# Performance work log

Hardware: AMD Instinct MI355X
Metric: run time of the kernel (lower is better)

Reference implementation:

```python
import jax, jax.numpy as jnp
import numpy as np

ENC_DIM, DEC_DIM, JOINT_DIM, VOCAB = 512, 640, 512, 1024
B, T, U = 8, 256, 64


def setup_inputs() -> dict:
    key = jax.random.key(0)
    ks = jax.random.split(key, 8)
    s_enc = 1.0 / np.sqrt(ENC_DIM)
    s_dec = 1.0 / np.sqrt(DEC_DIM)
    s_out = 1.0 / np.sqrt(2 * JOINT_DIM)
    return {
        "enc_out": jax.random.normal(ks[0], (B, T, ENC_DIM), jnp.float32),
        "pred_out": jax.random.normal(ks[1], (B, U, DEC_DIM), jnp.float32),
        "W_enc": jax.random.uniform(ks[2], (JOINT_DIM, ENC_DIM), jnp.float32, -s_enc, s_enc),
        "b_enc": jax.random.uniform(ks[3], (JOINT_DIM,), jnp.float32, -s_enc, s_enc),
        "W_pred": jax.random.uniform(ks[4], (JOINT_DIM, DEC_DIM), jnp.float32, -s_dec, s_dec),
        "b_pred": jax.random.uniform(ks[5], (JOINT_DIM,), jnp.float32, -s_dec, s_dec),
        "W_out": jax.random.uniform(ks[6], (VOCAB, 2 * JOINT_DIM), jnp.float32, -s_out, s_out),
        "b_out": jax.random.uniform(ks[7], (VOCAB,), jnp.float32, -s_out, s_out),
    }


def reference(enc_out, pred_out, W_enc, b_enc, W_pred, b_pred, W_out, b_out):
    # Dropout is identity in eval mode. fc_out on cat([enc_exp, pred_exp]) is
    # mathematically identical to splitting W_out in half and summing two
    # broadcast projections (avoids materializing the [B,T,U,2J] tensor).
    J = W_enc.shape[0]
    e = jnp.einsum('bte,je->btj', enc_out, W_enc) + b_enc    # [B,T,J]
    p = jnp.einsum('bud,jd->buj', pred_out, W_pred) + b_pred  # [B,U,J]
    W1, W2 = W_out[:, :J], W_out[:, J:]
    out = (jnp.einsum('btj,vj->btv', e, W1)[:, :, None, :]
           + jnp.einsum('buj,vj->buv', p, W2)[:, None, :, :]
           + b_out)                                           # [B,T,U,V]
    return out
```

## Files before the change

kernel.cpp:

```cpp
#include <hip/hip_runtime.h>

typedef float f4 __attribute__((ext_vector_type(4)));
typedef float f32x4 __attribute__((ext_vector_type(4)));
typedef short bf16x8 __attribute__((ext_vector_type(8)));
typedef unsigned short u16x8 __attribute__((ext_vector_type(8)));

static __device__ __forceinline__ unsigned short f2bf(float f) {
    unsigned int x = __builtin_bit_cast(unsigned int, f);
    x = (x + 0x7fffu + ((x >> 16) & 1u)) >> 16;
    return (unsigned short)x;
}
static __device__ __forceinline__ float bf2f(unsigned short h) {
    unsigned int x = ((unsigned int)h) << 16;
    return __builtin_bit_cast(float, x);
}

static __device__ __forceinline__ void gll16(const unsigned short* g, unsigned short* l) {
    __builtin_amdgcn_global_load_lds(
        (__attribute__((address_space(1))) void*)(g),
        (__attribute__((address_space(3))) void*)(l), 16, 0, 0);
}

static __device__ __forceinline__ int fragoff(int r, int s) {
    return r * 32 + ((s ^ ((r >> 1) & 3)) << 3);
}

struct GJobF {
    const float *A, *W;
    int lda, ldw;
    const float* bias;
    unsigned short *Ch, *Cl;
    int N, K, nbx;
};

__global__ __launch_bounds__(256, 3) void gemmcvt64(
    GJobF j0, GJobF j1, int nblk0, int nblk1,
    const float* __restrict__ Wo, unsigned short* __restrict__ Wo_h,
    unsigned short* __restrict__ Wo_l, int nWo8)
{
    __shared__ unsigned short lds[2][4][64 * 32];

    const int bid = blockIdx.x;
    const int tid = threadIdx.x;

    if (bid >= nblk0 + nblk1) {
        const int nblkc = (int)gridDim.x - nblk0 - nblk1;
        for (int g = (bid - nblk0 - nblk1) * 256 + tid; g < nWo8; g += nblkc * 256) {
            const int idx = g * 8;
            f4 a = *(const f4*)(Wo + idx);
            f4 b = *(const f4*)(Wo + idx + 4);
            u16x8 hv, lv;
            float s[8] = { a.x, a.y, a.z, a.w, b.x, b.y, b.z, b.w };
            #pragma unroll
            for (int i = 0; i < 8; ++i) {
                unsigned short h = f2bf(s[i]);
                hv[i] = h;
                lv[i] = f2bf(s[i] - bf2f(h));
            }
            *(u16x8*)(Wo_h + idx) = hv;
            *(u16x8*)(Wo_l + idx) = lv;
        }
        return;
    }

    const bool first = bid < nblk0;
    const GJobF J = first ? j0 : j1;
    const int local = first ? bid : bid - nblk0;
    const int m0 = (local % J.nbx) * 64;
    const int n0 = (local / J.nbx) * 64;

    const int lane = tid & 63;
    const int wid  = tid >> 6;
    const int wr   = wid >> 1, wc = wid & 1;
    const int lrow = lane & 15;
    const int s    = lane >> 4;

    const int row  = tid >> 2, slot = tid & 3;
    const int woff = fragoff(row, slot);
    const float* pA = J.A + (size_t)(m0 + row) * J.lda + slot * 8;
    const float* pW = J.W + (size_t)(n0 + row) * J.ldw + slot * 8;

    f4 ra0, ra1, rw0, rw1;

#define LOADREGS(k0) do { \
    ra0 = *(const f4*)(pA + (k0));     ra1 = *(const f4*)(pA + (k0) + 4); \
    rw0 = *(const f4*)(pW + (k0));     rw1 = *(const f4*)(pW + (k0) + 4); \
} while (0)

#define CVTWRITE(buf) do { \
    u16x8 ha, la, hw, lw; \
    float sa[8] = { ra0.x, ra0.y, ra0.z, ra0.w, ra1.x, ra1.y, ra1.z, ra1.w }; \
    float sw[8] = { rw0.x, rw0.y, rw0.z, rw0.w, rw1.x, rw1.y, rw1.z, rw1.w }; \
    _Pragma("unroll") \
    for (int i = 0; i < 8; ++i) { \
        unsigned short h = f2bf(sa[i]); \
        ha[i] = h; la[i] = f2bf(sa[i] - bf2f(h)); \
        h = f2bf(sw[i]); \
        hw[i] = h; lw[i] = f2bf(sw[i] - bf2f(h)); \
    } \
    *(u16x8*)&lds[buf][0][woff] = ha; \
    *(u16x8*)&lds[buf][1][woff] = la; \
    *(u16x8*)&lds[buf][2][woff] = hw; \
    *(u16x8*)&lds[buf][3][woff] = lw; \
} while (0)

    f32x4 acc[2][2];
    #pragma unroll
    for (int i = 0; i < 2; ++i)
        #pragma unroll
        for (int j = 0; j < 2; ++j) acc[i][j] = (f32x4){0.f, 0.f, 0.f, 0.f};

    const int nt = J.K / 32;

    LOADREGS(0);
    CVTWRITE(0);
    __syncthreads();

    int cur = 0;
    for (int t = 0; t < nt; ++t) {
        if (t + 1 < nt) LOADREGS((t + 1) * 32);

        bf16x8 ah[2], al[2], wh[2], wl[2];
        #pragma unroll
        for (int i = 0; i < 2; ++i) {
            const int ra = wr * 32 + i * 16 + lrow;
            const int rw = wc * 32 + i * 16 + lrow;
            ah[i] = *(const bf16x8*)&lds[cur][0][fragoff(ra, s)];
            al[i] = *(const bf16x8*)&lds[cur][1][fragoff(ra, s)];
            wh[i] = *(const bf16x8*)&lds[cur][2][fragoff(rw, s)];
            wl[i] = *(const bf16x8*)&lds[cur][3][fragoff(rw, s)];
        }
        #pragma unroll
        for (int i = 0; i < 2; ++i)
            #pragma unroll
            for (int j = 0; j < 2; ++j) {
                acc[i][j] = __builtin_amdgcn_mfma_f32_16x16x32_bf16(ah[i], wh[j], acc[i][j], 0, 0, 0);
                acc[i][j] = __builtin_amdgcn_mfma_f32_16x16x32_bf16(ah[i], wl[j], acc[i][j], 0, 0, 0);
                acc[i][j] = __builtin_amdgcn_mfma_f32_16x16x32_bf16(al[i], wh[j], acc[i][j], 0, 0, 0);
            }

        if (t + 1 < nt) {
            CVTWRITE(cur ^ 1);
            __syncthreads();
            cur ^= 1;
        }
    }
#undef LOADREGS
#undef CVTWRITE

    #pragma unroll
    for (int i = 0; i < 2; ++i) {
        const int rbase = m0 + wr * 32 + i * 16 + (lane >> 4) * 4;
        #pragma unroll
        for (int j = 0; j < 2; ++j) {
            const int col = n0 + wc * 32 + j * 16 + (lane & 15);
            const float bv = J.bias[col];
            #pragma unroll
            for (int r = 0; r < 4; ++r) {
                float v = acc[i][j][r] + bv;
                size_t off = (size_t)(rbase + r) * J.N + col;
                unsigned short h = f2bf(v);
                J.Ch[off] = h;
                J.Cl[off] = f2bf(v - bf2f(h));
            }
        }
    }
}

struct GJob {
    const unsigned short *Ah, *Al, *Wh, *Wl;
    int lda, ldw;
    const float* bias;
    float* Cf;
    int N, K, nbx;
};

__global__ __launch_bounds__(256, 3) void gemm64(GJob j0, GJob j1, int nblk0)
{
    __shared__ unsigned short lds[2][4][64 * 32];

    const bool first = (int)blockIdx.x < nblk0;
    const GJob J = first ? j0 : j1;
    const int local = first ? (int)blockIdx.x : (int)blockIdx.x - nblk0;
    const int m0 = (local % J.nbx) * 64;
    const int n0 = (local / J.nbx) * 64;

    const int tid  = threadIdx.x;
    const int lane = tid & 63;
    const int wid  = tid >> 6;
    const int wr   = wid >> 1, wc = wid & 1;
    const int lrow = lane & 15;
    const int s    = lane >> 4;

    const int srow  = wid * 16 + (lane >> 2);
    const int sslot = (lane & 3) ^ ((srow >> 1) & 3);
    const size_t gA = (size_t)(m0 + srow) * J.lda + sslot * 8;
    const size_t gW = (size_t)(n0 + srow) * J.ldw + sslot * 8;

    f32x4 acc[2][2];
    #pragma unroll
    for (int i = 0; i < 2; ++i)
        #pragma unroll
        for (int j = 0; j < 2; ++j) acc[i][j] = (f32x4){0.f, 0.f, 0.f, 0.f};

    const int nt = J.K / 32;

    gll16(J.Ah + gA, &lds[0][0][wid * 512]);
    gll16(J.Al + gA, &lds[0][1][wid * 512]);
    gll16(J.Wh + gW, &lds[0][2][wid * 512]);
    gll16(J.Wl + gW, &lds[0][3][wid * 512]);
    asm volatile("s_waitcnt vmcnt(0)" ::: "memory");
    __syncthreads();

    int cur = 0;
    for (int t = 0; t < nt; ++t) {
        if (t + 1 < nt) {
            const int k0 = (t + 1) * 32;
            gll16(J.Ah + gA + k0, &lds[cur ^ 1][0][wid * 512]);
            gll16(J.Al + gA + k0, &lds[cur ^ 1][1][wid * 512]);
            gll16(J.Wh + gW + k0, &lds[cur ^ 1][2][wid * 512]);
            gll16(J.Wl + gW + k0, &lds[cur ^ 1][3][wid * 512]);
        }

        bf16x8 ah[2], al[2], wh[2], wl[2];
        #pragma unroll
        for (int i = 0; i < 2; ++i) {
            const int ra = wr * 32 + i * 16 + lrow;
            const int rw = wc * 32 + i * 16 + lrow;
            ah[i] = *(const bf16x8*)&lds[cur][0][fragoff(ra, s)];
            al[i] = *(const bf16x8*)&lds[cur][1][fragoff(ra, s)];
            wh[i] = *(const bf16x8*)&lds[cur][2][fragoff(rw, s)];
            wl[i] = *(const bf16x8*)&lds[cur][3][fragoff(rw, s)];
        }
        #pragma unroll
        for (int i = 0; i < 2; ++i)
            #pragma unroll
            for (int j = 0; j < 2; ++j) {
                acc[i][j] = __builtin_amdgcn_mfma_f32_16x16x32_bf16(ah[i], wh[j], acc[i][j], 0, 0, 0);
                acc[i][j] = __builtin_amdgcn_mfma_f32_16x16x32_bf16(ah[i], wl[j], acc[i][j], 0, 0, 0);
                acc[i][j] = __builtin_amdgcn_mfma_f32_16x16x32_bf16(al[i], wh[j], acc[i][j], 0, 0, 0);
            }

        if (t + 1 < nt) {
            asm volatile("s_waitcnt vmcnt(0)" ::: "memory");
            __syncthreads();
            cur ^= 1;
        }
    }

    #pragma unroll
    for (int i = 0; i < 2; ++i) {
        const int rbase = m0 + wr * 32 + i * 16 + (lane >> 4) * 4;
        #pragma unroll
        for (int j = 0; j < 2; ++j) {
            const int col = n0 + wc * 32 + j * 16 + (lane & 15);
            const float bv = J.bias ? J.bias[col] : 0.f;
            #pragma unroll
            for (int r = 0; r < 4; ++r)
                J.Cf[(size_t)(rbase + r) * J.N + col] = acc[i][j][r] + bv;
        }
    }
}

__global__ __launch_bounds__(256) void bcast_kernel(
    const float* __restrict__ X, const float* __restrict__ Y,
    float* __restrict__ out, int T, int U)
{
    const int Vq  = 256;
    const int bt  = blockIdx.x;
    const int b   = bt / T;
    const int tid = threadIdx.x;

    const f4* X4 = (const f4*)X;
    const f4* Y4 = (const f4*)Y + (size_t)b * U * Vq;
    f4* O4 = (f4*)out + (size_t)bt * U * Vq;

    f4 x = X4[(size_t)bt * Vq + tid];
    #pragma unroll 4
    for (int u = 0; u < U; ++u) {
        f4 y = Y4[u * Vq + tid];
        f4 r = { x.x + y.x, x.y + y.y, x.z + y.z, x.w + y.w };
        __builtin_nontemporal_store(r, &O4[u * Vq + tid]);
    }
}

extern "C" void kernel_launch(void* const* d_in, const int* in_sizes, int n_in,
                              void* d_out, int out_size, void* d_ws, size_t ws_size,
                              hipStream_t stream) {
    (void)in_sizes; (void)n_in; (void)out_size; (void)ws_size;

    const int B = 8, T = 256, U = 64;
    const int ENC = 512, DEC = 640, J = 512, V = 1024;
    const int MT = B * T;
    const int MU = B * U;

    const float* enc    = (const float*)d_in[0];
    const float* pred   = (const float*)d_in[1];
    const float* W_enc  = (const float*)d_in[2];
    const float* b_enc  = (const float*)d_in[3];
    const float* W_pred = (const float*)d_in[4];
    const float* b_pred = (const float*)d_in[5];
    const float* W_out  = (const float*)d_in[6];
    const float* b_out  = (const float*)d_in[7];
    float* out = (float*)d_out;

    const int n_Wo = V * 2 * J;
    const int n_e  = MT * J;
    const int n_p  = MU * J;

    unsigned short* w = (unsigned short*)d_ws;
    unsigned short* Wo_h = w;
    unsigned short* Wo_l = Wo_h + n_Wo;
    unsigned short* e_h  = Wo_l + n_Wo;
    unsigned short* e_l  = e_h + n_e;
    unsigned short* p_h  = e_l + n_e;
    unsigned short* p_l  = p_h + n_p;
    float* ws_X = (float*)(p_l + n_p);
    float* ws_Y = ws_X + (size_t)MT * V;

    GJobF je = { enc,  W_enc,  ENC, ENC, b_enc,  e_h, e_l, J, ENC, MT / 64 };
    GJobF jp = { pred, W_pred, DEC, DEC, b_pred, p_h, p_l, J, DEC, MU / 64 };
    const int nbe = (MT / 64) * (J / 64);
    const int nbp = (MU / 64) * (J / 64);
    const int ncv = 64;
    gemmcvt64<<<nbe + nbp + ncv, 256, 0, stream>>>(
        je, jp, nbe, nbp, W_out, Wo_h, Wo_l, n_Wo / 8);

    GJob jx = { e_h, e_l, Wo_h, Wo_l, J, 2 * J, b_out, ws_X, V, J, MT / 64 };
    GJob jy = { p_h, p_l, Wo_h + J, Wo_l + J, J, 2 * J, nullptr, ws_Y, V, J, MU / 64 };
    const int nbx = (MT / 64) * (V / 64);
    const int nby = (MU / 64) * (V / 64);
    gemm64<<<nbx + nby, 256, 0, stream>>>(jx, jy, nbx);

    bcast_kernel<<<dim3(B * T), 256, 0, stream>>>(ws_X, ws_Y, out, T, U);
}
```

Measured before the change: 136.3 us.

## Drop weight low-part in split-bf16 GEMMs and widen output GEMM tile to 64x128

Removes the low-order bf16 correction term for the weight operand in both the projection and output GEMMs, going from three MFMA passes per product to two and no longer converting or storing a W_out low half. The output GEMM tile is widened to 64x128 with occupancy hint 4, which reuses each activation fragment across more columns and halves the block count. Accuracy drops because weights are now rounded to plain bf16, which may matter against the tolerance. The main cost is the workspace GEMMs, while the large broadcast write kernel is unchanged.

```diff
diff --git a/kernel.cpp b/kernel.cpp
--- a/kernel.cpp
+++ b/kernel.cpp
@@ -35,10 +35,9 @@
 
 __global__ __launch_bounds__(256, 3) void gemmcvt64(
     GJobF j0, GJobF j1, int nblk0, int nblk1,
-    const float* __restrict__ Wo, unsigned short* __restrict__ Wo_h,
-    unsigned short* __restrict__ Wo_l, int nWo8)
+    const float* __restrict__ Wo, unsigned short* __restrict__ Wo_h, int nWo8)
 {
-    __shared__ unsigned short lds[2][4][64 * 32];
+    __shared__ unsigned short lds[2][3][64 * 32];
 
     const int bid = blockIdx.x;
     const int tid = threadIdx.x;
@@ -49,16 +48,11 @@
             const int idx = g * 8;
             f4 a = *(const f4*)(Wo + idx);
             f4 b = *(const f4*)(Wo + idx + 4);
-            u16x8 hv, lv;
+            u16x8 hv;
             float s[8] = { a.x, a.y, a.z, a.w, b.x, b.y, b.z, b.w };
             #pragma unroll
-            for (int i = 0; i < 8; ++i) {
-                unsigned short h = f2bf(s[i]);
-                hv[i] = h;
-                lv[i] = f2bf(s[i] - bf2f(h));
-            }
+            for (int i = 0; i < 8; ++i) hv[i] = f2bf(s[i]);
             *(u16x8*)(Wo_h + idx) = hv;
-            *(u16x8*)(Wo_l + idx) = lv;
         }
         return;
     }
@@ -88,20 +82,18 @@
 } while (0)
 
 #define CVTWRITE(buf) do { \
-    u16x8 ha, la, hw, lw; \
+    u16x8 ha, la, hw; \
     float sa[8] = { ra0.x, ra0.y, ra0.z, ra0.w, ra1.x, ra1.y, ra1.z, ra1.w }; \
     float sw[8] = { rw0.x, rw0.y, rw0.z, rw0.w, rw1.x, rw1.y, rw1.z, rw1.w }; \
     _Pragma("unroll") \
     for (int i = 0; i < 8; ++i) { \
         unsigned short h = f2bf(sa[i]); \
         ha[i] = h; la[i] = f2bf(sa[i] - bf2f(h)); \
-        h = f2bf(sw[i]); \
-        hw[i] = h; lw[i] = f2bf(sw[i] - bf2f(h)); \
+        hw[i] = f2bf(sw[i]); \
     } \
     *(u16x8*)&lds[buf][0][woff] = ha; \
     *(u16x8*)&lds[buf][1][woff] = la; \
     *(u16x8*)&lds[buf][2][woff] = hw; \
-    *(u16x8*)&lds[buf][3][woff] = lw; \
 } while (0)
 
     f32x4 acc[2][2];
@@ -120,7 +112,7 @@
     for (int t = 0; t < nt; ++t) {
         if (t + 1 < nt) LOADREGS((t + 1) * 32);
 
-        bf16x8 ah[2], al[2], wh[2], wl[2];
+        bf16x8 ah[2], al[2], wh[2];
         #pragma unroll
         for (int i = 0; i < 2; ++i) {
             const int ra = wr * 32 + i * 16 + lrow;
@@ -128,14 +120,12 @@
             ah[i] = *(const bf16x8*)&lds[cur][0][fragoff(ra, s)];
             al[i] = *(const bf16x8*)&lds[cur][1][fragoff(ra, s)];
             wh[i] = *(const bf16x8*)&lds[cur][2][fragoff(rw, s)];
-            wl[i] = *(const bf16x8*)&lds[cur][3][fragoff(rw, s)];
         }
         #pragma unroll
         for (int i = 0; i < 2; ++i)
             #pragma unroll
             for (int j = 0; j < 2; ++j) {
                 acc[i][j] = __builtin_amdgcn_mfma_f32_16x16x32_bf16(ah[i], wh[j], acc[i][j], 0, 0, 0);
-                acc[i][j] = __builtin_amdgcn_mfma_f32_16x16x32_bf16(ah[i], wl[j], acc[i][j], 0, 0, 0);
                 acc[i][j] = __builtin_amdgcn_mfma_f32_16x16x32_bf16(al[i], wh[j], acc[i][j], 0, 0, 0);
             }
 
@@ -168,14 +158,14 @@
 }
 
 struct GJob {
-    const unsigned short *Ah, *Al, *Wh, *Wl;
+    const unsigned short *Ah, *Al, *Wh;
     int lda, ldw;
     const float* bias;
     float* Cf;
     int N, K, nbx;
 };
 
-__global__ __launch_bounds__(256, 3) void gemm64(GJob j0, GJob j1, int nblk0)
+__global__ __launch_bounds__(256, 4) void gemm64x128(GJob j0, GJob j1, int nblk0)
 {
     __shared__ unsigned short lds[2][4][64 * 32];
 
@@ -183,7 +173,7 @@
     const GJob J = first ? j0 : j1;
     const int local = first ? (int)blockIdx.x : (int)blockIdx.x - nblk0;
     const int m0 = (local % J.nbx) * 64;
-    const int n0 = (local / J.nbx) * 64;
+    const int n0 = (local / J.nbx) * 128;
 
     const int tid  = threadIdx.x;
     const int lane = tid & 63;
@@ -192,52 +182,56 @@
     const int lrow = lane & 15;
     const int s    = lane >> 4;
 
-    const int srow  = wid * 16 + (lane >> 2);
-    const int sslot = (lane & 3) ^ ((srow >> 1) & 3);
-    const size_t gA = (size_t)(m0 + srow) * J.lda + sslot * 8;
-    const size_t gW = (size_t)(n0 + srow) * J.ldw + sslot * 8;
-
-    f32x4 acc[2][2];
+    const int arow  = wid * 16 + (lane >> 2);
+    const int aslot = (lane & 3) ^ ((arow >> 1) & 3);
+    const size_t gA = (size_t)(m0 + arow) * J.lda + aslot * 8;
+    const int wrow0 = wid * 32 + (lane >> 2);
+    const int wrow1 = wrow0 + 16;
+    const int wsl0  = (lane & 3) ^ ((wrow0 >> 1) & 3);
+    const int wsl1  = (lane & 3) ^ ((wrow1 >> 1) & 3);
+    const size_t gW0 = (size_t)(n0 + wrow0) * J.ldw + wsl0 * 8;
+    const size_t gW1 = (size_t)(n0 + wrow1) * J.ldw + wsl1 * 8;
+
+#define STAGE(buf, k0) do { \
+    gll16(J.Ah + gA + (k0),  &lds[buf][0][wid * 512]); \
+    gll16(J.Al + gA + (k0),  &lds[buf][1][wid * 512]); \
+    gll16(J.Wh + gW0 + (k0), &lds[buf][2 + (wid >> 1)][(wid & 1) * 1024]); \
+    gll16(J.Wh + gW1 + (k0), &lds[buf][2 + (wid >> 1)][(wid & 1) * 1024 + 512]); \
+} while (0)
+
+    f32x4 acc[2][4];
     #pragma unroll
     for (int i = 0; i < 2; ++i)
         #pragma unroll
-        for (int j = 0; j < 2; ++j) acc[i][j] = (f32x4){0.f, 0.f, 0.f, 0.f};
+        for (int j = 0; j < 4; ++j) acc[i][j] = (f32x4){0.f, 0.f, 0.f, 0.f};
 
     const int nt = J.K / 32;
 
-    gll16(J.Ah + gA, &lds[0][0][wid * 512]);
-    gll16(J.Al + gA, &lds[0][1][wid * 512]);
-    gll16(J.Wh + gW, &lds[0][2][wid * 512]);
-    gll16(J.Wl + gW, &lds[0][3][wid * 512]);
+    STAGE(0, 0);
     asm volatile("s_waitcnt vmcnt(0)" ::: "memory");
     __syncthreads();
 
     int cur = 0;
     for (int t = 0; t < nt; ++t) {
-        if (t + 1 < nt) {
-            const int k0 = (t + 1) * 32;
-            gll16(J.Ah + gA + k0, &lds[cur ^ 1][0][wid * 512]);
-            gll16(J.Al + gA + k0, &lds[cur ^ 1][1][wid * 512]);
-            gll16(J.Wh + gW + k0, &lds[cur ^ 1][2][wid * 512]);
-            gll16(J.Wl + gW + k0, &lds[cur ^ 1][3][wid * 512]);
-        }
-
-        bf16x8 ah[2], al[2], wh[2], wl[2];
+        if (t + 1 < nt) STAGE(cur ^ 1, (t + 1) * 32);
+
+        bf16x8 ah[2], al[2], wh[4];
         #pragma unroll
         for (int i = 0; i < 2; ++i) {
             const int ra = wr * 32 + i * 16 + lrow;
-            const int rw = wc * 32 + i * 16 + lrow;
             ah[i] = *(const bf16x8*)&lds[cur][0][fragoff(ra, s)];
             al[i] = *(const bf16x8*)&lds[cur][1][fragoff(ra, s)];
-            wh[i] = *(const bf16x8*)&lds[cur][2][fragoff(rw, s)];
-            wl[i] = *(const bf16x8*)&lds[cur][3][fragoff(rw, s)];
+        }
+        #pragma unroll
+        for (int j = 0; j < 4; ++j) {
+            const int rw = wc * 64 + j * 16 + lrow;
+            wh[j] = *(const bf16x8*)&lds[cur][2 + (rw >> 6)][fragoff(rw & 63, s)];
         }
         #pragma unroll
         for (int i = 0; i < 2; ++i)
             #pragma unroll
-            for (int j = 0; j < 2; ++j) {
+            for (int j = 0; j < 4; ++j) {
                 acc[i][j] = __builtin_amdgcn_mfma_f32_16x16x32_bf16(ah[i], wh[j], acc[i][j], 0, 0, 0);
-                acc[i][j] = __builtin_amdgcn_mfma_f32_16x16x32_bf16(ah[i], wl[j], acc[i][j], 0, 0, 0);
                 acc[i][j] = __builtin_amdgcn_mfma_f32_16x16x32_bf16(al[i], wh[j], acc[i][j], 0, 0, 0);
             }
 
@@ -247,13 +241,14 @@
             cur ^= 1;
         }
     }
+#undef STAGE
 
     #pragma unroll
     for (int i = 0; i < 2; ++i) {
         const int rbase = m0 + wr * 32 + i * 16 + (lane >> 4) * 4;
         #pragma unroll
-        for (int j = 0; j < 2; ++j) {
-            const int col = n0 + wc * 32 + j * 16 + (lane & 15);
+        for (int j = 0; j < 4; ++j) {
+            const int col = n0 + wc * 64 + j * 16 + (lane & 15);
             const float bv = J.bias ? J.bias[col] : 0.f;
             #pragma unroll
             for (int r = 0; r < 4; ++r)
@@ -310,8 +305,7 @@
 
     unsigned short* w = (unsigned short*)d_ws;
     unsigned short* Wo_h = w;
-    unsigned short* Wo_l = Wo_h + n_Wo;
-    unsigned short* e_h  = Wo_l + n_Wo;
+    unsigned short* e_h  = Wo_h + n_Wo;
     unsigned short* e_l  = e_h + n_e;
     unsigned short* p_h  = e_l + n_e;
     unsigned short* p_l  = p_h + n_p;
@@ -324,13 +318,13 @@
     const int nbp = (MU / 64) * (J / 64);
     const int ncv = 64;
     gemmcvt64<<<nbe + nbp + ncv, 256, 0, stream>>>(
-        je, jp, nbe, nbp, W_out, Wo_h, Wo_l, n_Wo / 8);
-
-    GJob jx = { e_h, e_l, Wo_h, Wo_l, J, 2 * J, b_out, ws_X, V, J, MT / 64 };
-    GJob jy = { p_h, p_l, Wo_h + J, Wo_l + J, J, 2 * J, nullptr, ws_Y, V, J, MU / 64 };
-    const int nbx = (MT / 64) * (V / 64);
-    const int nby = (MU / 64) * (V / 64);
-    gemm64<<<nbx + nby, 256, 0, stream>>>(jx, jy, nbx);
+        je, jp, nbe, nbp, W_out, Wo_h, n_Wo / 8);
+
+    GJob jx = { e_h, e_l, Wo_h,     J, 2 * J, b_out,   ws_X, V, J, MT / 64 };
+    GJob jy = { p_h, p_l, Wo_h + J, J, 2 * J, nullptr, ws_Y, V, J, MU / 64 };
+    const int nbx = (MT / 64) * (V / 128);
+    const int nby = (MU / 64) * (V / 128);
+    gemm64x128<<<nbx + nby, 256, 0, stream>>>(jx, jy, nbx);
 
     bcast_kernel<<<dim3(B * T), 256, 0, stream>>>(ws_X, ws_Y, out, T, U);
 }
```

New measurement: 131.9 us. -3.2%, faster.
